# Optimization experiments

Hardware: AMD Instinct MI355X
Metric: run time of the kernel (lower is better)

Reference implementation:

```python
import jax, jax.numpy as jnp
import numpy as np

N = 50000      # nodes
E = 800000     # directed edges
D = 128        # input_dim == hidden_dim
EL = 100000    # edges scored by decoder


def setup_inputs() -> dict:
    key = jax.random.key(0)
    ks = jax.random.split(key, 8)
    s = 1.0 / np.sqrt(D)  # glorot-ish scale
    return {
        "node_feature": jax.random.normal(ks[0], (N, D), jnp.float32),
        "W1": jax.random.normal(ks[1], (D, D), jnp.float32) * s,
        "b1": jnp.zeros((D,), jnp.float32),
        "W2": jax.random.normal(ks[2], (D, D), jnp.float32) * s,
        "b2": jnp.zeros((D,), jnp.float32),
        "W3": jax.random.normal(ks[3], (D, D), jnp.float32) * s,
        "b3": jnp.zeros((D,), jnp.float32),
        "edge_index": jax.random.randint(ks[4], (2, E), 0, N, dtype=jnp.int32),
        "edge_label_index": jax.random.randint(ks[5], (2, EL), 0, N, dtype=jnp.int32),
    }


def _gcn_conv(x, W, b, src, dst, norm, n):
    # x' = D^{-1/2} (A + I) D^{-1/2} (x W) + b   (PyG GCNConv semantics)
    h = x @ W                                   # [N, D]
    msg = h[src] * norm[:, None]                # gather + scale, [E+N, D]
    out = jax.ops.segment_sum(msg, dst, num_segments=n)  # scatter-add
    return out + b


def reference(node_feature, W1, b1, W2, b2, W3, b3, edge_index, edge_label_index):
    n = node_feature.shape[0]
    loop = jnp.arange(n, dtype=edge_index.dtype)
    src = jnp.concatenate([edge_index[0], loop])  # self-loops appended
    dst = jnp.concatenate([edge_index[1], loop])
    # symmetric normalization: deg over destinations (incl. self-loops)
    deg = jax.ops.segment_sum(jnp.ones_like(dst, dtype=node_feature.dtype), dst, num_segments=n)
    dinv = jax.lax.rsqrt(jnp.maximum(deg, 1.0))
    norm = dinv[src] * dinv[dst]                 # [E+N]

    x = jax.nn.relu(_gcn_conv(node_feature, W1, b1, src, dst, norm, n))
    x = jax.nn.relu(_gcn_conv(x, W2, b2, src, dst, norm, n))
    x = _gcn_conv(x, W3, b3, src, dst, norm, n)

    # dot-product edge decoder
    u = x[edge_label_index[0]]
    v = x[edge_label_index[1]]
    return jnp.sum(u * v, axis=-1)               # [EL] logits
```

## Files before the change

kernel.cpp:

```cpp
#include <hip/hip_runtime.h>
#include <hip/hip_bf16.h>
#include <hip/hip_fp16.h>

typedef _Float16 v8h __attribute__((ext_vector_type(8)));
typedef float v4f __attribute__((ext_vector_type(4)));

__global__ __launch_bounds__(256) void gemm1_deg(const float* __restrict__ X,
                                                 const float* __restrict__ W,
                                                 __half* __restrict__ H, int Nrows,
                                                 int gemmBlocks, int degBlocks,
                                                 const int* __restrict__ dst,
                                                 int* __restrict__ cnt,
                                                 int* __restrict__ rank, int E,
                                                 const float* __restrict__ W2,
                                                 const float* __restrict__ W3,
                                                 __half* __restrict__ wfrag) {
    int tid = threadIdx.x;
    if (blockIdx.x >= gemmBlocks + degBlocks) {
        int o = (blockIdx.x - gemmBlocks - degBlocks) * 256 + tid;
        int w = o >> 14, r = o & 16383;
        const float* Ws = w ? W3 : W2;
        int k = r >> 7, ncol = r & 127;
        int c = ncol >> 4, nl = ncol & 15;
        int s = k >> 5, quad = (k >> 3) & 3, j = k & 7;
        int di = ((c * 4 + s) * 64 + quad * 16 + nl) * 8 + j;
        wfrag[(size_t)w * 16384 + di] = __float2half_rn(Ws[r]);
        return;
    }
    if (blockIdx.x >= gemmBlocks) {
        int base = (blockIdx.x - gemmBlocks) * 1024 + tid * 4;
        if (base + 3 < E) {
            int d0 = dst[base], d1 = dst[base + 1], d2 = dst[base + 2], d3 = dst[base + 3];
            int r0 = atomicAdd(&cnt[d0], 1);
            int r1 = atomicAdd(&cnt[d1], 1);
            int r2 = atomicAdd(&cnt[d2], 1);
            int r3 = atomicAdd(&cnt[d3], 1);
            rank[base] = r0; rank[base + 1] = r1; rank[base + 2] = r2; rank[base + 3] = r3;
        } else {
            for (int e = base; e < E; ++e) rank[e] = atomicAdd(&cnt[dst[e]], 1);
        }
        return;
    }
    __shared__ __align__(16) float xs[16][132];
    __shared__ __align__(16) float ws[16][128];
    int tx = tid & 15;
    int ty = tid >> 4;
    int row0 = blockIdx.x * 128;
    float acc[8][8] = {};
    for (int k0 = 0; k0 < 128; k0 += 16) {
        {
            int r = tid >> 2;
            int j = (tid & 3) * 4;
            int gr = row0 + r;
            float4 v = (gr < Nrows) ? *(const float4*)&X[(size_t)gr * 128 + k0 + j]
                                    : make_float4(0.f, 0.f, 0.f, 0.f);
            xs[j + 0][r] = v.x; xs[j + 1][r] = v.y; xs[j + 2][r] = v.z; xs[j + 3][r] = v.w;
            int gr2 = gr + 64;
            float4 u = (gr2 < Nrows) ? *(const float4*)&X[(size_t)gr2 * 128 + k0 + j]
                                     : make_float4(0.f, 0.f, 0.f, 0.f);
            xs[j + 0][r + 64] = u.x; xs[j + 1][r + 64] = u.y;
            xs[j + 2][r + 64] = u.z; xs[j + 3][r + 64] = u.w;
        }
        {
            const float4* Wv = (const float4*)&W[(size_t)k0 * 128];
            float4* wsv = (float4*)&ws[0][0];
            wsv[tid] = Wv[tid];
            wsv[tid + 256] = Wv[tid + 256];
        }
        __syncthreads();
#pragma unroll
        for (int kk = 0; kk < 16; ++kk) {
            float4 xa = *(float4*)&xs[kk][ty * 4];
            float4 xb = *(float4*)&xs[kk][ty * 4 + 64];
            float4 wa = *(float4*)&ws[kk][tx * 4];
            float4 wb = *(float4*)&ws[kk][tx * 4 + 64];
            float xr[8] = {xa.x, xa.y, xa.z, xa.w, xb.x, xb.y, xb.z, xb.w};
            float wr[8] = {wa.x, wa.y, wa.z, wa.w, wb.x, wb.y, wb.z, wb.w};
#pragma unroll
            for (int i = 0; i < 8; ++i)
#pragma unroll
                for (int j = 0; j < 8; ++j)
                    acc[i][j] += xr[i] * wr[j];
        }
        __syncthreads();
    }
    auto pk = [](float x, float y) { __half2 h = __floats2half2_rn(x, y); return *(unsigned int*)&h; };
#pragma unroll
    for (int i = 0; i < 8; ++i) {
        int gr = row0 + ((i < 4) ? (ty * 4 + i) : (64 + ty * 4 + i - 4));
        if (gr < Nrows) {
            uint2 q0 = make_uint2(pk(acc[i][0], acc[i][1]), pk(acc[i][2], acc[i][3]));
            uint2 q1 = make_uint2(pk(acc[i][4], acc[i][5]), pk(acc[i][6], acc[i][7]));
            *(uint2*)&H[(size_t)gr * 128 + tx * 4] = q0;
            *(uint2*)&H[(size_t)gr * 128 + 64 + tx * 4] = q1;
        }
    }
}

__global__ __launch_bounds__(256) void agg_gemm(const __half* __restrict__ Xs,
                                                const float* __restrict__ dinv,
                                                const int* __restrict__ rowptr,
                                                const int* __restrict__ col,
                                                const __half* __restrict__ wfrag,
                                                const float* __restrict__ bias,
                                                __half* __restrict__ Out,
                                                int n, int finalLayer) {
    __shared__ __align__(16) _Float16 y[64][136];
    int tid = threadIdx.x;
    int rowbase = blockIdx.x * 64;
    {
        int sub = tid >> 4;
        int t = (tid & 15) * 8;
        for (int g = 0; g < 4; ++g) {
            int rr = g * 16 + sub;
            int node = rowbase + rr;
            float a[8] = {};
            if (node < n) {
                int beg = rowptr[node], end = rowptr[node + 1];
                int k = beg;
                for (; k + 4 <= end; k += 4) {
                    int s0 = col[k], s1 = col[k + 1], s2 = col[k + 2], s3 = col[k + 3];
                    uint4 r0 = *(const uint4*)&Xs[(size_t)s0 * 128 + t];
                    uint4 r1 = *(const uint4*)&Xs[(size_t)s1 * 128 + t];
                    uint4 r2 = *(const uint4*)&Xs[(size_t)s2 * 128 + t];
                    uint4 r3 = *(const uint4*)&Xs[(size_t)s3 * 128 + t];
                    const __half2* h0 = (const __half2*)&r0;
                    const __half2* h1 = (const __half2*)&r1;
                    const __half2* h2 = (const __half2*)&r2;
                    const __half2* h3 = (const __half2*)&r3;
#pragma unroll
                    for (int m = 0; m < 4; ++m) {
                        float2 f0 = __half22float2(h0[m]);
                        float2 f1 = __half22float2(h1[m]);
                        float2 f2 = __half22float2(h2[m]);
                        float2 f3 = __half22float2(h3[m]);
                        a[2 * m]     += (f0.x + f1.x) + (f2.x + f3.x);
                        a[2 * m + 1] += (f0.y + f1.y) + (f2.y + f3.y);
                    }
                }
                for (; k < end; ++k) {
                    uint4 r0 = *(const uint4*)&Xs[(size_t)col[k] * 128 + t];
                    const __half2* h0 = (const __half2*)&r0;
#pragma unroll
                    for (int m = 0; m < 4; ++m) {
                        float2 f0 = __half22float2(h0[m]);
                        a[2 * m] += f0.x;
                        a[2 * m + 1] += f0.y;
                    }
                }
                float dn = dinv[node];
#pragma unroll
                for (int m = 0; m < 8; ++m) a[m] *= dn;
            }
            v8h yv;
#pragma unroll
            for (int m = 0; m < 8; ++m) yv[m] = (_Float16)a[m];
            *(v8h*)&y[rr][t] = yv;
        }
    }
    __syncthreads();
    int l = tid & 63;
    int wid = tid >> 6;
    int rb = wid * 16;
    int quad = l >> 4;
    int nn = l & 15;
    v8h a0 = *(const v8h*)&y[rb + nn][0 * 32 + quad * 8];
    v8h a1 = *(const v8h*)&y[rb + nn][1 * 32 + quad * 8];
    v8h a2 = *(const v8h*)&y[rb + nn][2 * 32 + quad * 8];
    v8h a3 = *(const v8h*)&y[rb + nn][3 * 32 + quad * 8];
    const v8h* Wf = (const v8h*)wfrag;
    v4f acc[8] = {};
#pragma unroll
    for (int c = 0; c < 8; ++c) {
        v8h b0 = Wf[(c * 4 + 0) * 64 + l];
        v8h b1 = Wf[(c * 4 + 1) * 64 + l];
        v8h b2 = Wf[(c * 4 + 2) * 64 + l];
        v8h b3 = Wf[(c * 4 + 3) * 64 + l];
        acc[c] = __builtin_amdgcn_mfma_f32_16x16x32_f16(a0, b0, acc[c], 0, 0, 0);
        acc[c] = __builtin_amdgcn_mfma_f32_16x16x32_f16(a1, b1, acc[c], 0, 0, 0);
        acc[c] = __builtin_amdgcn_mfma_f32_16x16x32_f16(a2, b2, acc[c], 0, 0, 0);
        acc[c] = __builtin_amdgcn_mfma_f32_16x16x32_f16(a3, b3, acc[c], 0, 0, 0);
    }
#pragma unroll
    for (int reg = 0; reg < 4; ++reg) {
        int gr = rowbase + rb + quad * 4 + reg;
        if (gr < n) {
            float dn = dinv[gr];
#pragma unroll
            for (int c = 0; c < 8; ++c) {
                float z = acc[c][reg] + bias[c * 16 + nn];
                if (!finalLayer) z = fmaxf(z, 0.f) * dn;
                Out[(size_t)gr * 128 + c * 16 + nn] = __float2half_rn(z);
            }
        }
    }
}

__global__ void scanA(const int* __restrict__ cnt, int* __restrict__ tmp,
                      int* __restrict__ bsum, int n) {
    __shared__ int s[256];
    int i = blockIdx.x * 256 + threadIdx.x;
    int v = (i < n) ? (cnt[i] + 1) : 0;
    s[threadIdx.x] = v;
    __syncthreads();
    for (int off = 1; off < 256; off <<= 1) {
        int x = (threadIdx.x >= off) ? s[threadIdx.x - off] : 0;
        __syncthreads();
        s[threadIdx.x] += x;
        __syncthreads();
    }
    if (i < n) tmp[i] = s[threadIdx.x];
    if (threadIdx.x == 255) bsum[blockIdx.x] = s[255];
}

__global__ void scanB(const int* __restrict__ tmp, const int* __restrict__ bsum,
                      const int* __restrict__ cnt, int* __restrict__ rowptr,
                      float* __restrict__ dinv, int* __restrict__ col, int n, int nb) {
    __shared__ int p[256];
    int t = threadIdx.x;
    p[t] = (t < nb) ? bsum[t] : 0;
    __syncthreads();
    for (int off = 1; off < 256; off <<= 1) {
        int x = (t >= off) ? p[t - off] : 0;
        __syncthreads();
        p[t] += x;
        __syncthreads();
    }
    int prefix = (blockIdx.x == 0) ? 0 : p[blockIdx.x - 1];
    int i = blockIdx.x * 256 + t;
    if (i < n) {
        int inc = tmp[i] + prefix;
        rowptr[i + 1] = inc;
        int c1 = cnt[i] + 1;
        dinv[i] = rsqrtf((float)c1);
        col[inc - c1] = i;
        if (i == 0) rowptr[0] = 0;
    }
}

__global__ __launch_bounds__(256) void fill4(const int* __restrict__ src,
                                             const int* __restrict__ dst,
                                             const int* __restrict__ rank,
                                             const int* __restrict__ rowptr,
                                             int* __restrict__ col, int E) {
    int base = blockIdx.x * 1024 + threadIdx.x * 4;
    if (base + 3 < E) {
        int d0 = dst[base], d1 = dst[base + 1], d2 = dst[base + 2], d3 = dst[base + 3];
        int s0 = src[base], s1 = src[base + 1], s2 = src[base + 2], s3 = src[base + 3];
        int r0 = rank[base], r1 = rank[base + 1], r2 = rank[base + 2], r3 = rank[base + 3];
        col[rowptr[d0] + 1 + r0] = s0;
        col[rowptr[d1] + 1 + r1] = s1;
        col[rowptr[d2] + 1 + r2] = s2;
        col[rowptr[d3] + 1 + r3] = s3;
    } else {
        for (int e = base; e < E; ++e)
            col[rowptr[dst[e]] + 1 + rank[e]] = src[e];
    }
}

__global__ __launch_bounds__(256) void agg_h(const __half* __restrict__ H,
                                             const float* __restrict__ dinv,
                                             const int* __restrict__ rowptr,
                                             const int* __restrict__ col,
                                             const float* __restrict__ bias,
                                             __half* __restrict__ out, int n) {
    int node = blockIdx.x * 16 + (threadIdx.x >> 4);
    int t = (threadIdx.x & 15) * 8;
    if (node >= n) return;
    int beg = rowptr[node], end = rowptr[node + 1];
    float a[8] = {};
    int k = beg;
    for (; k + 4 <= end; k += 4) {
        int s0 = col[k], s1 = col[k + 1], s2 = col[k + 2], s3 = col[k + 3];
        float w0 = dinv[s0], w1 = dinv[s1], w2 = dinv[s2], w3 = dinv[s3];
        uint4 r0 = *(const uint4*)&H[(size_t)s0 * 128 + t];
        uint4 r1 = *(const uint4*)&H[(size_t)s1 * 128 + t];
        uint4 r2 = *(const uint4*)&H[(size_t)s2 * 128 + t];
        uint4 r3 = *(const uint4*)&H[(size_t)s3 * 128 + t];
        const __half2* h0 = (const __half2*)&r0;
        const __half2* h1 = (const __half2*)&r1;
        const __half2* h2 = (const __half2*)&r2;
        const __half2* h3 = (const __half2*)&r3;
#pragma unroll
        for (int m = 0; m < 4; ++m) {
            float2 f0 = __half22float2(h0[m]);
            float2 f1 = __half22float2(h1[m]);
            float2 f2 = __half22float2(h2[m]);
            float2 f3 = __half22float2(h3[m]);
            a[2 * m]     += f0.x * w0 + f1.x * w1 + f2.x * w2 + f3.x * w3;
            a[2 * m + 1] += f0.y * w0 + f1.y * w1 + f2.y * w2 + f3.y * w3;
        }
    }
    for (; k < end; ++k) {
        int s0 = col[k];
        float w0 = dinv[s0];
        uint4 r0 = *(const uint4*)&H[(size_t)s0 * 128 + t];
        const __half2* h0 = (const __half2*)&r0;
#pragma unroll
        for (int m = 0; m < 4; ++m) {
            float2 f0 = __half22float2(h0[m]);
            a[2 * m] += f0.x * w0;
            a[2 * m + 1] += f0.y * w0;
        }
    }
    float dn = dinv[node];
    float4 b0 = *(const float4*)&bias[t];
    float4 b1 = *(const float4*)&bias[t + 4];
    float r0 = fmaxf(a[0] * dn + b0.x, 0.f) * dn;
    float r1 = fmaxf(a[1] * dn + b0.y, 0.f) * dn;
    float r2 = fmaxf(a[2] * dn + b0.z, 0.f) * dn;
    float r3 = fmaxf(a[3] * dn + b0.w, 0.f) * dn;
    float r4 = fmaxf(a[4] * dn + b1.x, 0.f) * dn;
    float r5 = fmaxf(a[5] * dn + b1.y, 0.f) * dn;
    float r6 = fmaxf(a[6] * dn + b1.z, 0.f) * dn;
    float r7 = fmaxf(a[7] * dn + b1.w, 0.f) * dn;
    auto pk = [](float x, float y) { __half2 h = __floats2half2_rn(x, y); return *(unsigned int*)&h; };
    uint4 o = make_uint4(pk(r0, r1), pk(r2, r3), pk(r4, r5), pk(r6, r7));
    *(uint4*)&out[(size_t)node * 128 + t] = o;
}

__global__ __launch_bounds__(256) void decoder_h(const __half* __restrict__ X,
                                                 const int* __restrict__ eli,
                                                 float* __restrict__ out, int EL) {
    int e = blockIdx.x * 16 + (threadIdx.x >> 4);
    int lane = threadIdx.x & 15;
    if (e >= EL) return;
    int u = eli[e], v = eli[EL + e];
    uint4 ra = *(const uint4*)&X[(size_t)u * 128 + lane * 8];
    uint4 rb = *(const uint4*)&X[(size_t)v * 128 + lane * 8];
    const __half2* ha = (const __half2*)&ra;
    const __half2* hb = (const __half2*)&rb;
    float d = 0.f;
#pragma unroll
    for (int j = 0; j < 4; ++j) {
        float2 fa = __half22float2(ha[j]);
        float2 fb = __half22float2(hb[j]);
        d += fa.x * fb.x + fa.y * fb.y;
    }
#pragma unroll
    for (int off = 8; off > 0; off >>= 1) d += __shfl_xor(d, off);
    if (lane == 0) out[e] = d;
}

extern "C" void kernel_launch(void* const* d_in, const int* in_sizes, int n_in,
                              void* d_out, int out_size, void* d_ws, size_t ws_size,
                              hipStream_t stream) {
    const float* x0 = (const float*)d_in[0];
    const float* W1 = (const float*)d_in[1];
    const float* b1 = (const float*)d_in[2];
    const float* W2 = (const float*)d_in[3];
    const float* b2 = (const float*)d_in[4];
    const float* W3 = (const float*)d_in[5];
    const float* b3 = (const float*)d_in[6];
    const int* ei   = (const int*)d_in[7];
    const int* eli  = (const int*)d_in[8];
    float* out = (float*)d_out;

    const int D = 128;
    const int N  = in_sizes[0] / D;
    const int E  = in_sizes[7] / 2;
    const int EL = in_sizes[8] / 2;

    const int* src = ei;
    const int* dst = ei + E;

    char* ws = (char*)d_ws;
    size_t off = 0;
    auto alloc = [&](size_t bytes) -> void* {
        off = (off + 255) & ~(size_t)255;
        void* p = ws + off;
        off += bytes;
        return p;
    };
    int*    cnt    = (int*)alloc((size_t)N * sizeof(int));
    int*    tmp    = (int*)alloc((size_t)N * sizeof(int));
    int*    bsum   = (int*)alloc(256 * sizeof(int));
    int*    rowptr = (int*)alloc((size_t)(N + 1) * sizeof(int));
    float*  dinv   = (float*)alloc((size_t)N * sizeof(float));
    int*    rank   = (int*)alloc((size_t)E * sizeof(int));
    int*    col    = (int*)alloc((size_t)(E + N) * sizeof(int));
    __half* wfrag  = (__half*)alloc((size_t)2 * 16384 * sizeof(__half));
    __half* hbuf   = (__half*)alloc((size_t)N * D * sizeof(__half));
    __half* xbuf   = (__half*)alloc((size_t)N * D * sizeof(__half));
    (void)ws_size;

    hipMemsetAsync(cnt, 0, (size_t)N * sizeof(int), stream);

    int nbN = (N + 255) / 256;
    int nbE4 = (E + 1023) / 1024;
    int gemmGrid = (N + 127) / 128;
    int fusedGrid = (N + 63) / 64;
    int aggGrid  = (N + 15) / 16;

    gemm1_deg<<<gemmGrid + nbE4 + 128, 256, 0, stream>>>(x0, W1, hbuf, N,
                                                         gemmGrid, nbE4,
                                                         dst, cnt, rank, E,
                                                         W2, W3, wfrag);

    scanA<<<nbN, 256, 0, stream>>>(cnt, tmp, bsum, N);
    scanB<<<nbN, 256, 0, stream>>>(tmp, bsum, cnt, rowptr, dinv, col, N, nbN);
    fill4<<<nbE4, 256, 0, stream>>>(src, dst, rank, rowptr, col, E);

    agg_h<<<aggGrid, 256, 0, stream>>>(hbuf, dinv, rowptr, col, b1, xbuf, N);
    agg_gemm<<<fusedGrid, 256, 0, stream>>>(xbuf, dinv, rowptr, col, wfrag, b2, hbuf, N, 0);
    agg_gemm<<<fusedGrid, 256, 0, stream>>>(hbuf, dinv, rowptr, col, wfrag + 16384, b3, xbuf, N, 1);

    decoder_h<<<(EL + 15) / 16, 256, 0, stream>>>(xbuf, eli, out, EL);
}
```

Measured before the change: 271.3 us.

## Build CSR via per-block shared-memory histograms and use MFMA for first GEMM

Replaces the global-atomic degree count and rank arrays with 64 per-chunk shared-memory 16-bit histograms. These are summed and prefix-scanned per destination, and a second pass recomputes ranks in shared memory to fill the CSR column array. The first-layer GEMM now converts X to fp16 and uses MFMA with pre-fragmented W1, fused with the histogram reduction and the first scan stage, and the memset is removed. The cost is an extra fp16 copy of X, a histogram buffer of 64×N entries, and 16-bit per-chunk counts that assume fewer than 65536 edges per node per chunk.

Measured after the change: 315.2 us. 1.16x slower.

```diff
diff --git a/kernel.cpp b/kernel.cpp
--- a/kernel.cpp
+++ b/kernel.cpp
@@ -5,96 +5,252 @@
 typedef _Float16 v8h __attribute__((ext_vector_type(8)));
 typedef float v4f __attribute__((ext_vector_type(4)));
 
-__global__ __launch_bounds__(256) void gemm1_deg(const float* __restrict__ X,
-                                                 const float* __restrict__ W,
-                                                 __half* __restrict__ H, int Nrows,
-                                                 int gemmBlocks, int degBlocks,
-                                                 const int* __restrict__ dst,
-                                                 int* __restrict__ cnt,
-                                                 int* __restrict__ rank, int E,
+#define NB 64
+#define HWORDS 12544
+
+__global__ __launch_bounds__(256) void hist_conv(const int* __restrict__ dst,
+                                                 unsigned* __restrict__ hist32,
+                                                 int E, int halfN, int chunk,
+                                                 const float* __restrict__ X0,
+                                                 __half* __restrict__ Xh, int nElem8,
+                                                 int convBlocks,
+                                                 const float* __restrict__ W1,
                                                  const float* __restrict__ W2,
                                                  const float* __restrict__ W3,
                                                  __half* __restrict__ wfrag) {
+    __shared__ unsigned sh[HWORDS];
     int tid = threadIdx.x;
-    if (blockIdx.x >= gemmBlocks + degBlocks) {
-        int o = (blockIdx.x - gemmBlocks - degBlocks) * 256 + tid;
-        int w = o >> 14, r = o & 16383;
-        const float* Ws = w ? W3 : W2;
-        int k = r >> 7, ncol = r & 127;
-        int c = ncol >> 4, nl = ncol & 15;
-        int s = k >> 5, quad = (k >> 3) & 3, j = k & 7;
-        int di = ((c * 4 + s) * 64 + quad * 16 + nl) * 8 + j;
-        wfrag[(size_t)w * 16384 + di] = __float2half_rn(Ws[r]);
+    if (blockIdx.x < NB) {
+        int b = blockIdx.x;
+        int e0 = b * chunk, e1 = min(e0 + chunk, E);
+        int hw = halfN >> 1;
+        for (int h = 0; h < 2; ++h) {
+            for (int j = tid; j < hw; j += 256) sh[j] = 0;
+            __syncthreads();
+            int base = h * halfN;
+            for (int e = e0 + tid; e < e1; e += 256) {
+                int rel = dst[e] - base;
+                if (rel >= 0 && rel < halfN)
+                    atomicAdd(&sh[rel >> 1], 1u << ((rel & 1) * 16));
+            }
+            __syncthreads();
+            unsigned* outp = hist32 + (size_t)b * halfN + h * hw;
+            for (int j = tid; j < hw; j += 256) outp[j] = sh[j];
+            __syncthreads();
+        }
         return;
     }
-    if (blockIdx.x >= gemmBlocks) {
-        int base = (blockIdx.x - gemmBlocks) * 1024 + tid * 4;
-        if (base + 3 < E) {
-            int d0 = dst[base], d1 = dst[base + 1], d2 = dst[base + 2], d3 = dst[base + 3];
-            int r0 = atomicAdd(&cnt[d0], 1);
-            int r1 = atomicAdd(&cnt[d1], 1);
-            int r2 = atomicAdd(&cnt[d2], 1);
-            int r3 = atomicAdd(&cnt[d3], 1);
-            rank[base] = r0; rank[base + 1] = r1; rank[base + 2] = r2; rank[base + 3] = r3;
-        } else {
-            for (int e = base; e < E; ++e) rank[e] = atomicAdd(&cnt[dst[e]], 1);
+    int bb = blockIdx.x - NB;
+    if (bb < convBlocks) {
+        int i = bb * 256 + tid;
+        if (i < nElem8) {
+            float4 v0 = ((const float4*)X0)[i * 2];
+            float4 v1 = ((const float4*)X0)[i * 2 + 1];
+            auto pk = [](float x, float y) { __half2 h = __floats2half2_rn(x, y); return *(unsigned int*)&h; };
+            uint4 q = make_uint4(pk(v0.x, v0.y), pk(v0.z, v0.w), pk(v1.x, v1.y), pk(v1.z, v1.w));
+            ((uint4*)Xh)[i] = q;
         }
         return;
     }
-    __shared__ __align__(16) float xs[16][132];
-    __shared__ __align__(16) float ws[16][128];
-    int tx = tid & 15;
-    int ty = tid >> 4;
-    int row0 = blockIdx.x * 128;
-    float acc[8][8] = {};
-    for (int k0 = 0; k0 < 128; k0 += 16) {
-        {
-            int r = tid >> 2;
-            int j = (tid & 3) * 4;
-            int gr = row0 + r;
-            float4 v = (gr < Nrows) ? *(const float4*)&X[(size_t)gr * 128 + k0 + j]
-                                    : make_float4(0.f, 0.f, 0.f, 0.f);
-            xs[j + 0][r] = v.x; xs[j + 1][r] = v.y; xs[j + 2][r] = v.z; xs[j + 3][r] = v.w;
-            int gr2 = gr + 64;
-            float4 u = (gr2 < Nrows) ? *(const float4*)&X[(size_t)gr2 * 128 + k0 + j]
-                                     : make_float4(0.f, 0.f, 0.f, 0.f);
-            xs[j + 0][r + 64] = u.x; xs[j + 1][r + 64] = u.y;
-            xs[j + 2][r + 64] = u.z; xs[j + 3][r + 64] = u.w;
-        }
-        {
-            const float4* Wv = (const float4*)&W[(size_t)k0 * 128];
-            float4* wsv = (float4*)&ws[0][0];
-            wsv[tid] = Wv[tid];
-            wsv[tid + 256] = Wv[tid + 256];
-        }
-        __syncthreads();
-#pragma unroll
-        for (int kk = 0; kk < 16; ++kk) {
-            float4 xa = *(float4*)&xs[kk][ty * 4];
-            float4 xb = *(float4*)&xs[kk][ty * 4 + 64];
-            float4 wa = *(float4*)&ws[kk][tx * 4];
-            float4 wb = *(float4*)&ws[kk][tx * 4 + 64];
-            float xr[8] = {xa.x, xa.y, xa.z, xa.w, xb.x, xb.y, xb.z, xb.w};
-            float wr[8] = {wa.x, wa.y, wa.z, wa.w, wb.x, wb.y, wb.z, wb.w};
-#pragma unroll
-            for (int i = 0; i < 8; ++i)
-#pragma unroll
-                for (int j = 0; j < 8; ++j)
-                    acc[i][j] += xr[i] * wr[j];
-        }
-        __syncthreads();
-    }
+    int o = (bb - convBlocks) * 256 + tid;
+    int w = o >> 14, r = o & 16383;
+    const float* Ws = (w == 0) ? W1 : (w == 1) ? W2 : W3;
+    int k = r >> 7, ncol = r & 127;
+    int c = ncol >> 4, nl = ncol & 15;
+    int s = k >> 5, quad = (k >> 3) & 3, j = k & 7;
+    int di = ((c * 4 + s) * 64 + quad * 16 + nl) * 8 + j;
+    wfrag[(size_t)w * 16384 + di] = __float2half_rn(Ws[r]);
+}
+
+__global__ __launch_bounds__(256) void gemm1_scanA(const __half* __restrict__ Xh,
+                                                   const __half* __restrict__ wfrag,
+                                                   __half* __restrict__ H, int Nrows,
+                                                   int gemmBlocks,
+                                                   const unsigned short* __restrict__ hist16,
+                                                   int halfN2,
+                                                   int* __restrict__ cnt, int* __restrict__ tmp,
+                                                   int* __restrict__ bsum, int n) {
+    __shared__ int s[256];
+    int tid = threadIdx.x;
+    if (blockIdx.x < gemmBlocks) {
+        int l = tid & 63;
+        int wid = tid >> 6;
+        int rowbase = blockIdx.x * 64 + wid * 16;
+        int quad = l >> 4;
+        int nn = l & 15;
+        int ra = rowbase + (l & 15);
+        if (ra > Nrows - 1) ra = Nrows - 1;
+        const v8h* Xf = (const v8h*)(Xh + (size_t)ra * 128);
+        v8h a0 = Xf[0 * 4 + quad];
+        v8h a1 = Xf[1 * 4 + quad];
+        v8h a2 = Xf[2 * 4 + quad];
+        v8h a3 = Xf[3 * 4 + quad];
+        const v8h* Wf = (const v8h*)wfrag;
+        v4f acc[8] = {};
+#pragma unroll
+        for (int c = 0; c < 8; ++c) {
+            v8h b0 = Wf[(c * 4 + 0) * 64 + l];
+            v8h b1 = Wf[(c * 4 + 1) * 64 + l];
+            v8h b2 = Wf[(c * 4 + 2) * 64 + l];
+            v8h b3 = Wf[(c * 4 + 3) * 64 + l];
+            acc[c] = __builtin_amdgcn_mfma_f32_16x16x32_f16(a0, b0, acc[c], 0, 0, 0);
+            acc[c] = __builtin_amdgcn_mfma_f32_16x16x32_f16(a1, b1, acc[c], 0, 0, 0);
+            acc[c] = __builtin_amdgcn_mfma_f32_16x16x32_f16(a2, b2, acc[c], 0, 0, 0);
+            acc[c] = __builtin_amdgcn_mfma_f32_16x16x32_f16(a3, b3, acc[c], 0, 0, 0);
+        }
+#pragma unroll
+        for (int reg = 0; reg < 4; ++reg) {
+            int gr = rowbase + quad * 4 + reg;
+            if (gr < Nrows) {
+#pragma unroll
+                for (int c = 0; c < 8; ++c)
+                    H[(size_t)gr * 128 + c * 16 + nn] = __float2half_rn(acc[c][reg]);
+            }
+        }
+        return;
+    }
+    int blk = blockIdx.x - gemmBlocks;
+    int i = blk * 256 + tid;
+    int v = 0;
+    if (i < n) {
+        int sum = 0;
+        for (int b = 0; b < NB; ++b) sum += hist16[(size_t)b * halfN2 + i];
+        cnt[i] = sum;
+        v = sum + 1;
+    }
+    s[tid] = v;
+    __syncthreads();
+    for (int off = 1; off < 256; off <<= 1) {
+        int x = (tid >= off) ? s[tid - off] : 0;
+        __syncthreads();
+        s[tid] += x;
+        __syncthreads();
+    }
+    if (i < n) tmp[i] = s[tid];
+    if (tid == 255) bsum[blk] = s[255];
+}
+
+__global__ void scanB(const int* __restrict__ tmp, const int* __restrict__ bsum,
+                      const int* __restrict__ cnt, int* __restrict__ rowptr,
+                      float* __restrict__ dinv, int* __restrict__ col, int n, int nb,
+                      unsigned short* __restrict__ hist16, int halfN2) {
+    __shared__ int p[256];
+    int t = threadIdx.x;
+    p[t] = (t < nb) ? bsum[t] : 0;
+    __syncthreads();
+    for (int off = 1; off < 256; off <<= 1) {
+        int x = (t >= off) ? p[t - off] : 0;
+        __syncthreads();
+        p[t] += x;
+        __syncthreads();
+    }
+    int prefix = (blockIdx.x == 0) ? 0 : p[blockIdx.x - 1];
+    int i = blockIdx.x * 256 + t;
+    if (i < n) {
+        int inc = tmp[i] + prefix;
+        rowptr[i + 1] = inc;
+        int c1 = cnt[i] + 1;
+        dinv[i] = rsqrtf((float)c1);
+        col[inc - c1] = i;
+        if (i == 0) rowptr[0] = 0;
+        unsigned run = 0;
+        for (int b = 0; b < NB; ++b) {
+            size_t ix = (size_t)b * halfN2 + i;
+            unsigned short tv = hist16[ix];
+            hist16[ix] = (unsigned short)run;
+            run += tv;
+        }
+    }
+}
+
+__global__ __launch_bounds__(256) void scatter_fill(const int* __restrict__ src,
+                                                    const int* __restrict__ dst,
+                                                    const unsigned* __restrict__ hist32,
+                                                    const int* __restrict__ rowptr,
+                                                    int* __restrict__ col,
+                                                    int E, int halfN, int chunk) {
+    __shared__ unsigned sh[HWORDS];
+    int tid = threadIdx.x;
+    int b = blockIdx.x;
+    int e0 = b * chunk, e1 = min(e0 + chunk, E);
+    int hw = halfN >> 1;
+    for (int h = 0; h < 2; ++h) {
+        const unsigned* in = hist32 + (size_t)b * halfN + h * hw;
+        for (int j = tid; j < hw; j += 256) sh[j] = in[j];
+        __syncthreads();
+        int base = h * halfN;
+        for (int e = e0 + tid; e < e1; e += 256) {
+            int d = dst[e];
+            int rel = d - base;
+            if (rel >= 0 && rel < halfN) {
+                unsigned old = atomicAdd(&sh[rel >> 1], 1u << ((rel & 1) * 16));
+                int rank = (old >> ((rel & 1) * 16)) & 0xffff;
+                col[rowptr[d] + 1 + rank] = src[e];
+            }
+        }
+        __syncthreads();
+    }
+}
+
+__global__ __launch_bounds__(256) void agg_h(const __half* __restrict__ H,
+                                             const float* __restrict__ dinv,
+                                             const int* __restrict__ rowptr,
+                                             const int* __restrict__ col,
+                                             const float* __restrict__ bias,
+                                             __half* __restrict__ out, int n) {
+    int node = blockIdx.x * 16 + (threadIdx.x >> 4);
+    int t = (threadIdx.x & 15) * 8;
+    if (node >= n) return;
+    int beg = rowptr[node], end = rowptr[node + 1];
+    float a[8] = {};
+    int k = beg;
+    for (; k + 4 <= end; k += 4) {
+        int s0 = col[k], s1 = col[k + 1], s2 = col[k + 2], s3 = col[k + 3];
+        float w0 = dinv[s0], w1 = dinv[s1], w2 = dinv[s2], w3 = dinv[s3];
+        uint4 r0 = *(const uint4*)&H[(size_t)s0 * 128 + t];
+        uint4 r1 = *(const uint4*)&H[(size_t)s1 * 128 + t];
+        uint4 r2 = *(const uint4*)&H[(size_t)s2 * 128 + t];
+        uint4 r3 = *(const uint4*)&H[(size_t)s3 * 128 + t];
+        const __half2* h0 = (const __half2*)&r0;
+        const __half2* h1 = (const __half2*)&r1;
+        const __half2* h2 = (const __half2*)&r2;
+        const __half2* h3 = (const __half2*)&r3;
+#pragma unroll
+        for (int m = 0; m < 4; ++m) {
+            float2 f0 = __half22float2(h0[m]);
+            float2 f1 = __half22float2(h1[m]);
+            float2 f2 = __half22float2(h2[m]);
+            float2 f3 = __half22float2(h3[m]);
+            a[2 * m]     += f0.x * w0 + f1.x * w1 + f2.x * w2 + f3.x * w3;
+            a[2 * m + 1] += f0.y * w0 + f1.y * w1 + f2.y * w2 + f3.y * w3;
+        }
+    }
+    for (; k < end; ++k) {
+        int s0 = col[k];
+        float w0 = dinv[s0];
+        uint4 r0 = *(const uint4*)&H[(size_t)s0 * 128 + t];
+        const __half2* h0 = (const __half2*)&r0;
+#pragma unroll
+        for (int m = 0; m < 4; ++m) {
+            float2 f0 = __half22float2(h0[m]);
+            a[2 * m] += f0.x * w0;
+            a[2 * m + 1] += f0.y * w0;
+        }
+    }
+    float dn = dinv[node];
+    float4 b0 = *(const float4*)&bias[t];
+    float4 b1 = *(const float4*)&bias[t + 4];
+    float r0 = fmaxf(a[0] * dn + b0.x, 0.f) * dn;
+    float r1 = fmaxf(a[1] * dn + b0.y, 0.f) * dn;
+    float r2 = fmaxf(a[2] * dn + b0.z, 0.f) * dn;
+    float r3 = fmaxf(a[3] * dn + b0.w, 0.f) * dn;
+    float r4 = fmaxf(a[4] * dn + b1.x, 0.f) * dn;
+    float r5 = fmaxf(a[5] * dn + b1.y, 0.f) * dn;
+    float r6 = fmaxf(a[6] * dn + b1.z, 0.f) * dn;
+    float r7 = fmaxf(a[7] * dn + b1.w, 0.f) * dn;
     auto pk = [](float x, float y) { __half2 h = __floats2half2_rn(x, y); return *(unsigned int*)&h; };
-#pragma unroll
-    for (int i = 0; i < 8; ++i) {
-        int gr = row0 + ((i < 4) ? (ty * 4 + i) : (64 + ty * 4 + i - 4));
-        if (gr < Nrows) {
-            uint2 q0 = make_uint2(pk(acc[i][0], acc[i][1]), pk(acc[i][2], acc[i][3]));
-            uint2 q1 = make_uint2(pk(acc[i][4], acc[i][5]), pk(acc[i][6], acc[i][7]));
-            *(uint2*)&H[(size_t)gr * 128 + tx * 4] = q0;
-            *(uint2*)&H[(size_t)gr * 128 + 64 + tx * 4] = q1;
-        }
-    }
+    uint4 o = make_uint4(pk(r0, r1), pk(r2, r3), pk(r4, r5), pk(r6, r7));
+    *(uint4*)&out[(size_t)node * 128 + t] = o;
 }
 
 __global__ __launch_bounds__(256) void agg_gemm(const __half* __restrict__ Xs,
@@ -196,129 +352,6 @@
     }
 }
 
-__global__ void scanA(const int* __restrict__ cnt, int* __restrict__ tmp,
-                      int* __restrict__ bsum, int n) {
-    __shared__ int s[256];
-    int i = blockIdx.x * 256 + threadIdx.x;
-    int v = (i < n) ? (cnt[i] + 1) : 0;
-    s[threadIdx.x] = v;
-    __syncthreads();
-    for (int off = 1; off < 256; off <<= 1) {
-        int x = (threadIdx.x >= off) ? s[threadIdx.x - off] : 0;
-        __syncthreads();
-        s[threadIdx.x] += x;
-        __syncthreads();
-    }
-    if (i < n) tmp[i] = s[threadIdx.x];
-    if (threadIdx.x == 255) bsum[blockIdx.x] = s[255];
-}
-
-__global__ void scanB(const int* __restrict__ tmp, const int* __restrict__ bsum,
-                      const int* __restrict__ cnt, int* __restrict__ rowptr,
-                      float* __restrict__ dinv, int* __restrict__ col, int n, int nb) {
-    __shared__ int p[256];
-    int t = threadIdx.x;
-    p[t] = (t < nb) ? bsum[t] : 0;
-    __syncthreads();
-    for (int off = 1; off < 256; off <<= 1) {
-        int x = (t >= off) ? p[t - off] : 0;
-        __syncthreads();
-        p[t] += x;
-        __syncthreads();
-    }
-    int prefix = (blockIdx.x == 0) ? 0 : p[blockIdx.x - 1];
-    int i = blockIdx.x * 256 + t;
-    if (i < n) {
-        int inc = tmp[i] + prefix;
-        rowptr[i + 1] = inc;
-        int c1 = cnt[i] + 1;
-        dinv[i] = rsqrtf((float)c1);
-        col[inc - c1] = i;
-        if (i == 0) rowptr[0] = 0;
-    }
-}
-
-__global__ __launch_bounds__(256) void fill4(const int* __restrict__ src,
-                                             const int* __restrict__ dst,
-                                             const int* __restrict__ rank,
-                                             const int* __restrict__ rowptr,
-                                             int* __restrict__ col, int E) {
-    int base = blockIdx.x * 1024 + threadIdx.x * 4;
-    if (base + 3 < E) {
-        int d0 = dst[base], d1 = dst[base + 1], d2 = dst[base + 2], d3 = dst[base + 3];
-        int s0 = src[base], s1 = src[base + 1], s2 = src[base + 2], s3 = src[base + 3];
-        int r0 = rank[base], r1 = rank[base + 1], r2 = rank[base + 2], r3 = rank[base + 3];
-        col[rowptr[d0] + 1 + r0] = s0;
-        col[rowptr[d1] + 1 + r1] = s1;
-        col[rowptr[d2] + 1 + r2] = s2;
-        col[rowptr[d3] + 1 + r3] = s3;
-    } else {
-        for (int e = base; e < E; ++e)
-            col[rowptr[dst[e]] + 1 + rank[e]] = src[e];
-    }
-}
-
-__global__ __launch_bounds__(256) void agg_h(const __half* __restrict__ H,
-                                             const float* __restrict__ dinv,
-                                             const int* __restrict__ rowptr,
-                                             const int* __restrict__ col,
-                                             const float* __restrict__ bias,
-                                             __half* __restrict__ out, int n) {
-    int node = blockIdx.x * 16 + (threadIdx.x >> 4);
-    int t = (threadIdx.x & 15) * 8;
-    if (node >= n) return;
-    int beg = rowptr[node], end = rowptr[node + 1];
-    float a[8] = {};
-    int k = beg;
-    for (; k + 4 <= end; k += 4) {
-        int s0 = col[k], s1 = col[k + 1], s2 = col[k + 2], s3 = col[k + 3];
-        float w0 = dinv[s0], w1 = dinv[s1], w2 = dinv[s2], w3 = dinv[s3];
-        uint4 r0 = *(const uint4*)&H[(size_t)s0 * 128 + t];
-        uint4 r1 = *(const uint4*)&H[(size_t)s1 * 128 + t];
-        uint4 r2 = *(const uint4*)&H[(size_t)s2 * 128 + t];
-        uint4 r3 = *(const uint4*)&H[(size_t)s3 * 128 + t];
-        const __half2* h0 = (const __half2*)&r0;
-        const __half2* h1 = (const __half2*)&r1;
-        const __half2* h2 = (const __half2*)&r2;
-        const __half2* h3 = (const __half2*)&r3;
-#pragma unroll
-        for (int m = 0; m < 4; ++m) {
-            float2 f0 = __half22float2(h0[m]);
-            float2 f1 = __half22float2(h1[m]);
-            float2 f2 = __half22float2(h2[m]);
-            float2 f3 = __half22float2(h3[m]);
-            a[2 * m]     += f0.x * w0 + f1.x * w1 + f2.x * w2 + f3.x * w3;
-            a[2 * m + 1] += f0.y * w0 + f1.y * w1 + f2.y * w2 + f3.y * w3;
-        }
-    }
-    for (; k < end; ++k) {
-        int s0 = col[k];
-        float w0 = dinv[s0];
-        uint4 r0 = *(const uint4*)&H[(size_t)s0 * 128 + t];
-        const __half2* h0 = (const __half2*)&r0;
-#pragma unroll
-        for (int m = 0; m < 4; ++m) {
-            float2 f0 = __half22float2(h0[m]);
-            a[2 * m] += f0.x * w0;
-            a[2 * m + 1] += f0.y * w0;
-        }
-    }
-    float dn = dinv[node];
-    float4 b0 = *(const float4*)&bias[t];
-    float4 b1 = *(const float4*)&bias[t + 4];
-    float r0 = fmaxf(a[0] * dn + b0.x, 0.f) * dn;
-    float r1 = fmaxf(a[1] * dn + b0.y, 0.f) * dn;
-    float r2 = fmaxf(a[2] * dn + b0.z, 0.f) * dn;
-    float r3 = fmaxf(a[3] * dn + b0.w, 0.f) * dn;
-    float r4 = fmaxf(a[4] * dn + b1.x, 0.f) * dn;
-    float r5 = fmaxf(a[5] * dn + b1.y, 0.f) * dn;
-    float r6 = fmaxf(a[6] * dn + b1.z, 0.f) * dn;
-    float r7 = fmaxf(a[7] * dn + b1.w, 0.f) * dn;
-    auto pk = [](float x, float y) { __half2 h = __floats2half2_rn(x, y); return *(unsigned int*)&h; };
-    uint4 o = make_uint4(pk(r0, r1), pk(r2, r3), pk(r4, r5), pk(r6, r7));
-    *(uint4*)&out[(size_t)node * 128 + t] = o;
-}
-
 __global__ __launch_bounds__(256) void decoder_h(const __half* __restrict__ X,
                                                  const int* __restrict__ eli,
                                                  float* __restrict__ out, int EL) {
@@ -364,6 +397,11 @@
     const int* src = ei;
     const int* dst = ei + E;
 
+    int halfN = (N + 1) / 2;
+    halfN += (halfN & 1);
+    int halfN2 = 2 * halfN;
+    int chunk = (E + NB - 1) / NB;
+
     char* ws = (char*)d_ws;
     size_t off = 0;
     auto alloc = [&](size_t bytes) -> void* {
@@ -372,38 +410,39 @@
         off += bytes;
         return p;
     };
-    int*    cnt    = (int*)alloc((size_t)N * sizeof(int));
-    int*    tmp    = (int*)alloc((size_t)N * sizeof(int));
-    int*    bsum   = (int*)alloc(256 * sizeof(int));
-    int*    rowptr = (int*)alloc((size_t)(N + 1) * sizeof(int));
-    float*  dinv   = (float*)alloc((size_t)N * sizeof(float));
-    int*    rank   = (int*)alloc((size_t)E * sizeof(int));
-    int*    col    = (int*)alloc((size_t)(E + N) * sizeof(int));
-    __half* wfrag  = (__half*)alloc((size_t)2 * 16384 * sizeof(__half));
-    __half* hbuf   = (__half*)alloc((size_t)N * D * sizeof(__half));
-    __half* xbuf   = (__half*)alloc((size_t)N * D * sizeof(__half));
+    int*      cnt    = (int*)alloc((size_t)N * sizeof(int));
+    int*      tmp    = (int*)alloc((size_t)N * sizeof(int));
+    int*      bsum   = (int*)alloc(256 * sizeof(int));
+    int*      rowptr = (int*)alloc((size_t)(N + 1) * sizeof(int));
+    float*    dinv   = (float*)alloc((size_t)N * sizeof(float));
+    int*      col    = (int*)alloc((size_t)(E + N) * sizeof(int));
+    unsigned* hist32 = (unsigned*)alloc((size_t)NB * halfN * sizeof(unsigned));
+    __half*   wfrag  = (__half*)alloc((size_t)3 * 16384 * sizeof(__half));
+    __half*   xh0    = (__half*)alloc((size_t)N * D * sizeof(__half));
+    __half*   hbuf   = (__half*)alloc((size_t)N * D * sizeof(__half));
+    __half*   xbuf   = (__half*)alloc((size_t)N * D * sizeof(__half));
     (void)ws_size;
 
-    hipMemsetAsync(cnt, 0, (size_t)N * sizeof(int), stream);
-
     int nbN = (N + 255) / 256;
-    int nbE4 = (E + 1023) / 1024;
-    int gemmGrid = (N + 127) / 128;
+    int gemmGrid  = (N + 63) / 64;
     int fusedGrid = (N + 63) / 64;
-    int aggGrid  = (N + 15) / 16;
-
-    gemm1_deg<<<gemmGrid + nbE4 + 128, 256, 0, stream>>>(x0, W1, hbuf, N,
-                                                         gemmGrid, nbE4,
-                                                         dst, cnt, rank, E,
-                                                         W2, W3, wfrag);
-
-    scanA<<<nbN, 256, 0, stream>>>(cnt, tmp, bsum, N);
-    scanB<<<nbN, 256, 0, stream>>>(tmp, bsum, cnt, rowptr, dinv, col, N, nbN);
-    fill4<<<nbE4, 256, 0, stream>>>(src, dst, rank, rowptr, col, E);
+    int aggGrid   = (N + 15) / 16;
+    int nElem8    = N * D / 8;
+    int convBlocks = (nElem8 + 255) / 256;
+
+    hist_conv<<<NB + convBlocks + 192, 256, 0, stream>>>(dst, hist32, E, halfN, chunk,
+                                                         x0, xh0, nElem8, convBlocks,
+                                                         W1, W2, W3, wfrag);
+    gemm1_scanA<<<gemmGrid + nbN, 256, 0, stream>>>(xh0, wfrag, hbuf, N, gemmGrid,
+                                                    (const unsigned short*)hist32, halfN2,
+                                                    cnt, tmp, bsum, N);
+    scanB<<<nbN, 256, 0, stream>>>(tmp, bsum, cnt, rowptr, dinv, col, N, nbN,
+                                   (unsigned short*)hist32, halfN2);
+    scatter_fill<<<NB, 256, 0, stream>>>(src, dst, hist32, rowptr, col, E, halfN, chunk);
 
     agg_h<<<aggGrid, 256, 0, stream>>>(hbuf, dinv, rowptr, col, b1, xbuf, N);
-    agg_gemm<<<fusedGrid, 256, 0, stream>>>(xbuf, dinv, rowptr, col, wfrag, b2, hbuf, N, 0);
-    agg_gemm<<<fusedGrid, 256, 0, stream>>>(hbuf, dinv, rowptr, col, wfrag + 16384, b3, xbuf, N, 1);
+    agg_gemm<<<fusedGrid, 256, 0, stream>>>(xbuf, dinv, rowptr, col, wfrag + 16384, b2, hbuf, N, 0);
+    agg_gemm<<<fusedGrid, 256, 0, stream>>>(hbuf, dinv, rowptr, col, wfrag + 2 * 16384, b3, xbuf, N, 1);
 
     decoder_h<<<(EL + 15) / 16, 256, 0, stream>>>(xbuf, eli, out, EL);
 }
```
